# Kernel tuning notes

Hardware: AMD Instinct MI355X
Metric: run time of the kernel (lower is better)

Reference implementation:

```python
import jax, jax.numpy as jnp
import numpy as np

NUM_PATCHES = 16
QPB = 20          # qubits per tree block
NBLOCKS = 4
N = 1 << QPB      # 2**20 amplitudes per block statevector
INV_SQRT2 = 0.7071067811865476


def _single_qubit_states(x, pos_weights):
    """H @ (data-encoding rotations) |0> for every wire, grouped into blocks.
    x: (B,16,4,3) color angles; pos_weights: (16,2). Returns (B,4,20,2) c64.
    The leading Hadamard of the layer-1 IQP unitary is folded in here since
    the pre-layer-1 state is a tensor product of single-qubit states."""
    B = x.shape[0]
    hx, hy, hz = 0.5 * x[..., 0], 0.5 * x[..., 1], 0.5 * x[..., 2]
    v0 = jnp.cos(hx) + 0j
    v1 = -1j * jnp.sin(hx)                       # RX|0>
    cy, sy = jnp.cos(hy), jnp.sin(hy)
    w0 = cy * v0 - sy * v1
    w1 = sy * v0 + cy * v1                       # RY
    pz = jnp.exp(-1j * hz)
    w0 = pz * w0
    w1 = jnp.conj(pz) * w1                       # RZ
    color = jnp.stack([w0 + w1, w0 - w1], -1) * INV_SQRT2       # H  -> (B,16,4,2)

    px, py = 0.5 * pos_weights[:, 0], 0.5 * pos_weights[:, 1]
    a0 = jnp.cos(px) + 0j
    a1 = -1j * jnp.sin(px)                       # RX|0>
    cy, sy = jnp.cos(py), jnp.sin(py)
    b0 = cy * a0 - sy * a1
    b1 = sy * a0 + cy * a1                       # RY
    anc = jnp.stack([b0 + b1, b0 - b1], -1) * INV_SQRT2         # (16,2)
    anc = jnp.broadcast_to(anc[None, :, None, :], (B, NUM_PATCHES, 1, 2))

    states = jnp.concatenate([color, anc], axis=2)              # (B,16,5,2)
    return states.reshape(B, NBLOCKS, QPB, 2).astype(jnp.complex64)


def _forward(x, pos_weights, layer_1_weights, layer_2_weights, head_w, head_b):
    B = x.shape[0]
    states = _single_qubit_states(x, pos_weights)   # (B,4,20,2)

    # Build each block's 2^20 product statevector (wire 0 = slowest index).
    psi = states[:, :, 0, :]
    for q in range(1, QPB):
        psi = (psi[..., None] * states[:, :, q][:, :, None, :]).reshape(B, NBLOCKS, -1)

    # Layer-1 diagonal: RZ(a_i) + ring IsingZZ(b_i); phase exp(-i/2 (a.z + b.(z*roll(z)))).
    idx = jnp.arange(N, dtype=jnp.uint32)
    shifts = (QPB - 1 - jnp.arange(QPB, dtype=jnp.uint32))
    z = 1.0 - 2.0 * ((idx[None, :] >> shifts[:, None]) & 1).astype(jnp.float32)  # (20,N)
    a1, b1 = layer_1_weights[:, 0], layer_1_weights[:, 1]
    theta = a1 @ z + b1 @ (z * jnp.roll(z, -1, axis=0))
    psi = psi * jnp.exp(-0.5j * theta).astype(jnp.complex64)

    # Closing Hadamard layer of layer-1 IQP = Walsh-Hadamard transform on 20 wires.
    for i in range(QPB):
        psi = psi.reshape(B, NBLOCKS, 1 << i, 2, 1 << (QPB - 1 - i))
        p0, p1 = psi[:, :, :, 0, :], psi[:, :, :, 1, :]
        psi = jnp.stack([p0 + p1, p0 - p1], axis=3) * INV_SQRT2
    psi = psi.reshape(B, NBLOCKS, N)

    # Reduced density matrix on the 4 surviving qubits (first 4 wires) of each block.
    A = psi.reshape(B, NBLOCKS, 16, N // 16)
    rho4 = jnp.einsum('bkim,bkjm->bkij', A, jnp.conj(A))        # (B,4,16,16)
    r = rho4.reshape(B, NBLOCKS, 2, 2, 2, 2, 2, 2, 2, 2)
    rho012 = jnp.einsum('bkpqrxstux->bkpqrstu', r).reshape(B, NBLOCKS, 8, 8)
    rho123 = jnp.einsum('bkxpqrxstu->bkpqrstu', r).reshape(B, NBLOCKS, 8, 8)
    rho01  = jnp.einsum('bkpqxystxy->bkpqst', r).reshape(B, NBLOCKS, 4, 4)
    rho23  = jnp.einsum('bkxypqxyst->bkpqst', r).reshape(B, NBLOCKS, 4, 4)
    rho_q0 = jnp.einsum('bkpxyzqxyz->bkpq', r)                  # (B,4,2,2)
    rho_q3 = jnp.einsum('bkxyzpxyzq->bkpq', r)

    # Layer-2 IQP (H D H) in Heisenberg picture: U2^dag Z_k U2 =
    #   Z_k exp(-i a_k X_k) exp(-i b_{k-1} X_{k-1} X_k) exp(-i b_k X_k X_{k+1}),
    # a 3-qubit operator on ring positions (k-1, k, k+1) of the 16 survivors.
    I2 = jnp.eye(2, dtype=jnp.complex64)
    X = jnp.array([[0, 1], [1, 0]], dtype=jnp.complex64)
    Z = jnp.array([[1, 0], [0, -1]], dtype=jnp.complex64)
    I8 = jnp.eye(8, dtype=jnp.complex64)
    IZI = jnp.kron(I2, jnp.kron(Z, I2))
    IXI = jnp.kron(I2, jnp.kron(X, I2))
    XXI = jnp.kron(X, jnp.kron(X, I2))
    IXX = jnp.kron(I2, jnp.kron(X, X))

    def rot(t, P):
        return jnp.cos(t) * I8 - 1j * jnp.sin(t) * P

    a2, b2 = layer_2_weights[:, 0], layer_2_weights[:, 1]

    def heis_op(k):
        return IZI @ rot(a2[k], IXI) @ rot(b2[(k - 1) % 16], XXI) @ rot(b2[k], IXX)

    def tr(O, rho):  # Re Tr[O rho] per batch element
        return jnp.real(jnp.einsum('ij,bji->b', O, rho))

    # Blocks are independent before layer 2 -> cross-block joints are tensor products.
    # Ring position 15 = block 3 survivor q3; position 4 = block 1 survivor q0.
    rho_k0 = jnp.einsum('bij,bkl->bikjl', rho_q3[:, 3], rho01[:, 0]).reshape(B, 8, 8)
    rho_k3 = jnp.einsum('bij,bkl->bikjl', rho23[:, 0], rho_q0[:, 1]).reshape(B, 8, 8)

    e0 = tr(heis_op(0), rho_k0)
    e1 = tr(heis_op(1), rho012[:, 0])
    e2 = tr(heis_op(2), rho123[:, 0])
    e3 = tr(heis_op(3), rho_k3)
    q_out = jnp.stack([e0, e1, e2, e3], axis=-1).astype(jnp.float32)  # (B,4)

    out = q_out @ head_w.T + head_b
    norm = jnp.linalg.norm(out, axis=-1, keepdims=True)
    return out / jnp.maximum(norm, 1e-12)


def setup_inputs() -> dict:
    key = jax.random.key(0)
    ks = jax.random.split(key, 6)
    B = 8
    x = jax.random.uniform(ks[0], (B, NUM_PATCHES, 4, 3), dtype=jnp.float32,
                           minval=0.0, maxval=np.pi)
    pos_weights = jax.random.normal(ks[1], (16, 2), dtype=jnp.float32) * 0.01
    layer_1_weights = jax.random.normal(ks[2], (20, 2), dtype=jnp.float32) * 0.1
    layer_2_weights = jax.random.normal(ks[3], (16, 2), dtype=jnp.float32) * 0.1
    head_w = jax.random.normal(ks[4], (512, 4), dtype=jnp.float32) * 0.1
    head_b = jax.random.normal(ks[5], (512,), dtype=jnp.float32) * 0.01
    return {'x': x, 'pos_weights': pos_weights, 'layer_1_weights': layer_1_weights,
            'layer_2_weights': layer_2_weights, 'head_w': head_w, 'head_b': head_b}


def reference(x, pos_weights, layer_1_weights, layer_2_weights, head_w, head_b):
    return _forward(x, pos_weights, layer_1_weights, layer_2_weights, head_w, head_b)
```

## Files before the change

### kernel.cpp

```cpp
#include <hip/hip_runtime.h>
#include <math.h>

#define INV_SQRT2F 0.70710678118654752f

__device__ __forceinline__ float2 cmul(float2 a, float2 b) {
  return make_float2(a.x*b.x - a.y*b.y, a.x*b.y + a.y*b.x);
}
__device__ __forceinline__ float2 cmulc(float2 a, float2 b) {
  return make_float2(a.x*b.x + a.y*b.y, a.y*b.x - a.x*b.y);
}
__device__ __forceinline__ float2 cadd(float2 a, float2 b) {
  return make_float2(a.x + b.x, a.y + b.y);
}

__global__ __launch_bounds__(1024) void iqp_fused_kernel(
    const float* __restrict__ x,
    const float* __restrict__ pw,
    const float* __restrict__ lw,
    const float* __restrict__ l2,
    const float* __restrict__ hw,
    const float* __restrict__ hb,
    float* __restrict__ out)
{
  const int b = blockIdx.x;
  const int t = threadIdx.x;
  const int lane = t & 63;
  const int wid = t >> 6;

  __shared__ float2 sqs[3][20][2];
  __shared__ float  b1s[20];
  __shared__ float2 W[3][4][8][33];
  __shared__ float2 D0[8][64];
  __shared__ float2 ipv[6];
  __shared__ float2 q3part[4][3];
  __shared__ float2 rho[256];
  __shared__ float2 r012[64], r123[64], rk0[64], rk3[64];
  __shared__ float2 r01[16], r23[16], q0s[4], q3s[4];
  __shared__ float  e[4];
  __shared__ float  wsum[8];
  __shared__ float  nrm;

  if (t < 60) {
    const int kidx = t / 20, q = t % 20;
    const int k = (kidx == 2) ? 3 : kidx;
    const int pch = 4*k + q/5;
    const int j = q % 5;
    float2 s0, s1;
    if (j < 4) {
      const float* xp = x + ((size_t)((b*16 + pch)*4 + j))*3;
      float cx, sx, cy, sy, cz, sz;
      __sincosf(0.5f*xp[0], &sx, &cx);
      __sincosf(0.5f*xp[1], &sy, &cy);
      __sincosf(0.5f*xp[2], &sz, &cz);
      float2 w0 = make_float2(cy*cx,  sy*sx);
      float2 w1 = make_float2(sy*cx, -cy*sx);
      w0 = cmul(make_float2(cz, -sz), w0);
      w1 = cmul(make_float2(cz,  sz), w1);
      s0 = make_float2((w0.x + w1.x)*INV_SQRT2F, (w0.y + w1.y)*INV_SQRT2F);
      s1 = make_float2((w0.x - w1.x)*INV_SQRT2F, (w0.y - w1.y)*INV_SQRT2F);
    } else {
      float cx, sx, cy, sy;
      __sincosf(0.5f*pw[2*pch], &sx, &cx);
      __sincosf(0.5f*pw[2*pch + 1], &sy, &cy);
      const float2 w0 = make_float2(cy*cx,  sy*sx);
      const float2 w1 = make_float2(sy*cx, -cy*sx);
      s0 = make_float2((w0.x + w1.x)*INV_SQRT2F, (w0.y + w1.y)*INV_SQRT2F);
      s1 = make_float2((w0.x - w1.x)*INV_SQRT2F, (w0.y - w1.y)*INV_SQRT2F);
    }
    float ca, sa;
    __sincosf(0.5f*lw[2*q], &sa, &ca);
    sqs[kidx][q][0] = cmul(s0, make_float2(ca, -sa));
    sqs[kidx][q][1] = cmul(s1, make_float2(ca,  sa));
    if (kidx == 0) b1s[q] = lw[2*q + 1];
  }
  __syncthreads();

  if (wid < 12) {
    const int kk = wid >> 2;
    const int cls = wid & 3;
    const int b0 = cls & 1, b9 = cls >> 1;

    int bq[10];
    bq[0] = b0; bq[9] = b9;
    #pragma unroll
    for (int q = 3; q < 9; ++q) bq[q] = (lane >> (8 - q)) & 1;

    float2 base = sqs[kk][0][b0];
    #pragma unroll
    for (int q = 3; q < 9; ++q) base = cmul(base, sqs[kk][q][bq[q]]);
    base = cmul(base, sqs[kk][9][b9]);
    {
      float phi = 0.f;
      #pragma unroll
      for (int q = 3; q < 9; ++q) {
        const float zq  = 1.f - 2.f*(float)bq[q];
        const float zq1 = 1.f - 2.f*(float)bq[q + 1];
        phi += b1s[q]*zq*zq1;
      }
      float sp, cp;
      __sincosf(0.5f*phi, &sp, &cp);
      base = cmul(base, make_float2(cp, -sp));
    }
    const float2 t0 = cmul(base, sqs[kk][1][0]);
    const float2 t1 = cmul(base, sqs[kk][1][1]);
    const float z0 = 1.f - 2.f*(float)b0;
    const float z3 = 1.f - 2.f*(float)bq[3];

    float2 v[4];
    #pragma unroll
    for (int j = 0; j < 4; ++j) {
      const int j1 = j >> 1, j0 = j & 1;
      const float z1 = 1.f - 2.f*(float)j1;
      const float z2 = 1.f - 2.f*(float)j0;
      const float phij = b1s[0]*z0*z1 + b1s[1]*z1*z2 + b1s[2]*z2*z3;
      float sp, cp;
      __sincosf(0.5f*phij, &sp, &cp);
      v[j] = cmul(cmul(j1 ? t1 : t0, sqs[kk][2][j0]), make_float2(cp, -sp));
    }

    if (kk != 1) {
      {
        float2 a0 = v[0], a2 = v[2];
        v[0] = cadd(a0, a2); v[2] = make_float2(a0.x - a2.x, a0.y - a2.y);
        float2 a1 = v[1], a3 = v[3];
        v[1] = cadd(a1, a3); v[3] = make_float2(a1.x - a3.x, a1.y - a3.y);
        a0 = v[0]; a1 = v[1];
        v[0] = cadd(a0, a1); v[1] = make_float2(a0.x - a1.x, a0.y - a1.y);
        a2 = v[2]; a3 = v[3];
        v[2] = cadd(a2, a3); v[3] = make_float2(a2.x - a3.x, a2.y - a3.y);
      }
      #pragma unroll
      for (int mask = 1; mask <= 32; mask <<= 1) {
        #pragma unroll
        for (int j = 0; j < 4; ++j) {
          const float px = __shfl_xor(v[j].x, mask);
          const float py = __shfl_xor(v[j].y, mask);
          if (lane & mask) v[j] = make_float2(px - v[j].x, py - v[j].y);
          else             v[j] = make_float2(v[j].x + px, v[j].y + py);
        }
      }
    }
    const float scl = (kk == 1) ? 1.0f : 0.0625f;
    #pragma unroll
    for (int j = 0; j < 4; ++j) {
      const int m = j*64 + lane;
      W[kk][cls][m >> 5][m & 31] =
          make_float2(v[j].x*scl, v[j].y*scl);
    }
  }
  __syncthreads();

  if (wid < 8) {
    const int pr = t >> 6, idx = t & 63, xx = idx >> 3, yy = idx & 7;
    const int pa = pr >> 1;
    const int pb = (pr & 1) + ((pr >> 2) << 1);
    float2 acc = make_float2(0.f, 0.f);
    #pragma unroll 8
    for (int u = 0; u < 32; ++u)
      acc = cadd(acc, cmulc(W[0][pa][xx][u], W[0][pb][yy][u]));
    D0[pr][xx*8 + yy] = acc;
  } else if (wid < 12) {
    const int w4 = wid - 8;
    const int prl[6][2] = {{0,0},{1,1},{2,2},{3,3},{0,1},{2,3}};
    #pragma unroll
    for (int rep = 0; rep < 2; ++rep) {
      const int which = (rep == 0) ? w4 : w4 + 4;
      if (rep == 1 && w4 >= 2) break;
      const int pa = prl[which][0], pb = prl[which][1];
      float2 acc = make_float2(0.f, 0.f);
      #pragma unroll
      for (int jj = 0; jj < 4; ++jj) {
        const int m = jj*64 + lane;
        acc = cadd(acc, cmulc(W[1][pa][m >> 5][m & 31],
                              W[1][pb][m >> 5][m & 31]));
      }
      for (int off = 32; off > 0; off >>= 1) {
        acc.x += __shfl_down(acc.x, off);
        acc.y += __shfl_down(acc.y, off);
      }
      if (lane == 0) ipv[which] = acc;
    }
  } else {
    const int c = wid - 12;
    const int lo = lane >> 4;
    const int u0 = (lane & 15)*2;
    float2 a00 = make_float2(0.f, 0.f), a01 = a00, a11 = a00;
    #pragma unroll
    for (int du = 0; du < 2; ++du) {
      const float2 p0 = W[2][c][(lo << 1)    ][u0 + du];
      const float2 p1 = W[2][c][(lo << 1) | 1][u0 + du];
      a00 = cadd(a00, cmulc(p0, p0));
      a01 = cadd(a01, cmulc(p0, p1));
      a11 = cadd(a11, cmulc(p1, p1));
    }
    for (int off = 32; off > 0; off >>= 1) {
      a00.x += __shfl_down(a00.x, off); a00.y += __shfl_down(a00.y, off);
      a01.x += __shfl_down(a01.x, off); a01.y += __shfl_down(a01.y, off);
      a11.x += __shfl_down(a11.x, off); a11.y += __shfl_down(a11.y, off);
    }
    if (lane == 0) {
      q3part[c][0] = a00; q3part[c][1] = a01; q3part[c][2] = a11;
    }
  }
  __syncthreads();

  if (t < 256) {
    const int i = t >> 4, j = t & 15;
    const int xy = (i & 7)*8 + (j & 7);
    const int si = i >> 3, sj = j >> 3;
    const float2 q19a = sqs[0][19][0], q19b = sqs[0][19][1];
    const float s19a = q19a.x*q19a.x + q19a.y*q19a.y;
    const float s19b = q19b.x*q19b.x + q19b.y*q19b.y;
    const float cb = __cosf(b1s[19]), sb = __sinf(b1s[19]);
    const float2 gam = make_float2((s19a + s19b)*cb, (s19b - s19a)*sb);
    float2 acc = cadd(D0[0][xy], D0[4][xy]);
    {
      const float2 t2 = cadd(D0[3][xy], D0[7][xy]);
      const float sg = ((si ^ sj) & 1) ? -1.f : 1.f;
      acc.x += sg*t2.x; acc.y += sg*t2.y;
    }
    {
      float2 t3 = cadd(D0[1][xy], D0[5][xy]);
      t3 = cmul(gam, t3);
      const float sg = (sj & 1) ? -1.f : 1.f;
      acc.x += sg*t3.x; acc.y += sg*t3.y;
    }
    {
      float2 t4 = cadd(D0[2][xy], D0[6][xy]);
      t4 = cmulc(t4, gam);
      const float sg = (si & 1) ? -1.f : 1.f;
      acc.x += sg*t4.x; acc.y += sg*t4.y;
    }
    rho[t] = make_float2(0.5f*acc.x, 0.5f*acc.y);
  } else if (t < 260) {
    const int pp = (t - 256) >> 1, qq = (t - 256) & 1;
    const float2 q19a = sqs[1][19][0], q19b = sqs[1][19][1];
    const float s19a = q19a.x*q19a.x + q19a.y*q19a.y;
    const float s19b = q19b.x*q19b.x + q19b.y*q19b.y;
    const float cb = __cosf(b1s[19]), sb = __sinf(b1s[19]);
    const float2 gam1 = make_float2((s19a + s19b)*cb, (s19b - s19a)*sb);
    const float2 T04 = cadd(ipv[0], ipv[2]);
    const float2 T37 = cadd(ipv[1], ipv[3]);
    const float2 T15 = cadd(ipv[4], ipv[5]);
    const float2 h = cmul(gam1, T15);
    float2 acc = T04;
    const float sg1 = ((pp ^ qq) & 1) ? -1.f : 1.f;
    acc.x += sg1*T37.x; acc.y += sg1*T37.y;
    const float sgq = (qq & 1) ? -1.f : 1.f;
    acc.x += sgq*h.x; acc.y += sgq*h.y;
    const float sgp = (pp & 1) ? -1.f : 1.f;
    acc.x += sgp*h.x; acc.y -= sgp*h.y;
    q0s[pp*2 + qq] = make_float2(0.5f*acc.x, 0.5f*acc.y);
  } else if (t < 264) {
    const int ei = t - 260;
    const int pp = ei >> 1, qq = ei & 1;
    const int src = (pp == 0 && qq == 0) ? 0 : (pp == 1 && qq == 1) ? 2 : 1;
    float2 s = make_float2(0.f, 0.f);
    #pragma unroll
    for (int c = 0; c < 4; ++c) s = cadd(s, q3part[c][src]);
    if (pp == 1 && qq == 0) s.y = -s.y;
    q3s[pp*2 + qq] = s;
  }
  __syncthreads();

  if (t < 64) {
    const int i = t >> 3, j = t & 7;
    r012[t] = cadd(rho[(2*i)*16 + 2*j], rho[(2*i + 1)*16 + 2*j + 1]);
    r123[t] = cadd(rho[i*16 + j], rho[(i + 8)*16 + (j + 8)]);
  }
  if (t >= 64 && t < 80) {
    const int tt = t - 64;
    const int i = tt >> 2, j = tt & 3;
    float2 s1 = make_float2(0.f, 0.f), s2 = make_float2(0.f, 0.f);
    #pragma unroll
    for (int w = 0; w < 4; ++w) {
      s1 = cadd(s1, rho[(4*i + w)*16 + 4*j + w]);
      s2 = cadd(s2, rho[(4*w + i)*16 + 4*w + j]);
    }
    r01[tt] = s1;  r23[tt] = s2;
  }
  __syncthreads();

  if (t < 64) {
    const int i = t >> 3, j = t & 7;
    rk0[t] = cmul(q3s[(i >> 2)*2 + (j >> 2)], r01[(i & 3)*4 + (j & 3)]);
    rk3[t] = cmul(r23[(i >> 1)*4 + (j >> 1)], q0s[(i & 1)*2 + (j & 1)]);
  }
  __syncthreads();

  if (t < 256) {
    const int k = t >> 6;
    const int idx = t & 63;
    const int i = idx >> 3, j = idx & 7;
    const float alpha = l2[2*k];
    const float beta1 = l2[2*((k + 15) & 15) + 1];
    const float beta2 = l2[2*k + 1];
    float ca, sa, cb1, sb1, cb2, sb2;
    __sincosf(alpha, &sa, &ca);
    __sincosf(beta1, &sb1, &cb1);
    __sincosf(beta2, &sb2, &cb2);
    float2 m1, m2;
    {
      const int xr = i ^ j;
      m1 = (xr == 0) ? make_float2( cb1*cb2, 0.f)
         : (xr == 3) ? make_float2( 0.f,    -cb1*sb2)
         : (xr == 6) ? make_float2( 0.f,    -sb1*cb2)
         : (xr == 5) ? make_float2(-sb1*sb2, 0.f)
         : make_float2(0.f, 0.f);
      const int xr2 = xr ^ 2;
      m2 = (xr2 == 0) ? make_float2( cb1*cb2, 0.f)
         : (xr2 == 3) ? make_float2( 0.f,    -cb1*sb2)
         : (xr2 == 6) ? make_float2( 0.f,    -sb1*cb2)
         : (xr2 == 5) ? make_float2(-sb1*sb2, 0.f)
         : make_float2(0.f, 0.f);
    }
    float2 O = make_float2(ca*m1.x + sa*m2.y, ca*m1.y - sa*m2.x);
    if ((i >> 1) & 1) { O.x = -O.x; O.y = -O.y; }
    const float2* rp = (k == 0) ? rk0 : (k == 1) ? r012 : (k == 2) ? r123 : rk3;
    const float2 rv = rp[j*8 + i];
    float contrib = O.x*rv.x - O.y*rv.y;
    for (int off = 32; off > 0; off >>= 1) contrib += __shfl_down(contrib, off);
    if (idx == 0) e[k] = contrib;
  }
  __syncthreads();

  float val = 0.f;
  if (t < 512) {
    val = hb[t] + e[0]*hw[4*t] + e[1]*hw[4*t + 1]
        + e[2]*hw[4*t + 2] + e[3]*hw[4*t + 3];
    float ss = val*val;
    for (int off = 32; off > 0; off >>= 1) ss += __shfl_down(ss, off);
    if ((t & 63) == 0) wsum[t >> 6] = ss;
  }
  __syncthreads();
  if (t == 0) {
    float s = 0.f;
    for (int w = 0; w < 8; ++w) s += wsum[w];
    nrm = fmaxf(sqrtf(s), 1e-12f);
  }
  __syncthreads();
  if (t < 512) out[(size_t)b*512 + t] = val / nrm;
}

extern "C" void kernel_launch(void* const* d_in, const int* in_sizes, int n_in,
                              void* d_out, int out_size, void* d_ws, size_t ws_size,
                              hipStream_t stream) {
  const float* x  = (const float*)d_in[0];
  const float* pw = (const float*)d_in[1];
  const float* lw = (const float*)d_in[2];
  const float* l2 = (const float*)d_in[3];
  const float* hw = (const float*)d_in[4];
  const float* hb = (const float*)d_in[5];
  const int B = in_sizes[0] / (16*4*3);

  iqp_fused_kernel<<<B, 1024, 0, stream>>>(x, pw, lw, l2, hw, hb, (float*)d_out);
}
```

Before: 69.30 us.

## Shrink block to 768 threads, hoist trig/gamma precompute, merge partial-trace stages

```diff
diff --git a/kernel.cpp b/kernel.cpp
--- a/kernel.cpp
+++ b/kernel.cpp
@@ -13,7 +13,7 @@
   return make_float2(a.x + b.x, a.y + b.y);
 }
 
-__global__ __launch_bounds__(1024) void iqp_fused_kernel(
+__global__ __launch_bounds__(768) void iqp_fused_kernel(
     const float* __restrict__ x,
     const float* __restrict__ pw,
     const float* __restrict__ lw,
@@ -29,13 +29,15 @@
 
   __shared__ float2 sqs[3][20][2];
   __shared__ float  b1s[20];
+  __shared__ float2 gams[2];
+  __shared__ float  trig[4][6];
   __shared__ float2 W[3][4][8][33];
   __shared__ float2 D0[8][64];
   __shared__ float2 ipv[6];
   __shared__ float2 q3part[4][3];
   __shared__ float2 rho[256];
   __shared__ float2 r012[64], r123[64], rk0[64], rk3[64];
-  __shared__ float2 r01[16], r23[16], q0s[4], q3s[4];
+  __shared__ float2 q0s[4], q3s[4];
   __shared__ float  e[4];
   __shared__ float  wsum[8];
   __shared__ float  nrm;
@@ -72,10 +74,29 @@
     sqs[kidx][q][0] = cmul(s0, make_float2(ca, -sa));
     sqs[kidx][q][1] = cmul(s1, make_float2(ca,  sa));
     if (kidx == 0) b1s[q] = lw[2*q + 1];
-  }
-  __syncthreads();
-
-  if (wid < 12) {
+    if (q == 19 && kidx < 2) {
+      const float m0 = s0.x*s0.x + s0.y*s0.y;
+      const float m1 = s1.x*s1.x + s1.y*s1.y;
+      float sb, cb;
+      __sincosf(lw[39], &sb, &cb);
+      gams[kidx] = make_float2((m0 + m1)*cb, (m1 - m0)*sb);
+    }
+  } else if (t >= 64 && t < 68) {
+    const int k = t - 64;
+    const float alpha = l2[2*k];
+    const float beta1 = l2[2*((k + 15) & 15) + 1];
+    const float beta2 = l2[2*k + 1];
+    float ca, sa, cb1, sb1, cb2, sb2;
+    __sincosf(alpha, &sa, &ca);
+    __sincosf(beta1, &sb1, &cb1);
+    __sincosf(beta2, &sb2, &cb2);
+    trig[k][0] = ca;  trig[k][1] = sa;
+    trig[k][2] = cb1; trig[k][3] = sb1;
+    trig[k][4] = cb2; trig[k][5] = sb2;
+  }
+  __syncthreads();
+
+  {
     const int kk = wid >> 2;
     const int cls = wid & 3;
     const int b0 = cls & 1, b9 = cls >> 1;
@@ -159,13 +180,12 @@
     for (int u = 0; u < 32; ++u)
       acc = cadd(acc, cmulc(W[0][pa][xx][u], W[0][pb][yy][u]));
     D0[pr][xx*8 + yy] = acc;
-  } else if (wid < 12) {
-    const int w4 = wid - 8;
+  } else if (wid < 10) {
+    const int u = wid - 8;
     const int prl[6][2] = {{0,0},{1,1},{2,2},{3,3},{0,1},{2,3}};
     #pragma unroll
-    for (int rep = 0; rep < 2; ++rep) {
-      const int which = (rep == 0) ? w4 : w4 + 4;
-      if (rep == 1 && w4 >= 2) break;
+    for (int rep = 0; rep < 3; ++rep) {
+      const int which = u*3 + rep;
       const int pa = prl[which][0], pb = prl[which][1];
       float2 acc = make_float2(0.f, 0.f);
       #pragma unroll
@@ -181,25 +201,29 @@
       if (lane == 0) ipv[which] = acc;
     }
   } else {
-    const int c = wid - 12;
+    const int u = wid - 10;
     const int lo = lane >> 4;
     const int u0 = (lane & 15)*2;
-    float2 a00 = make_float2(0.f, 0.f), a01 = a00, a11 = a00;
-    #pragma unroll
-    for (int du = 0; du < 2; ++du) {
-      const float2 p0 = W[2][c][(lo << 1)    ][u0 + du];
-      const float2 p1 = W[2][c][(lo << 1) | 1][u0 + du];
-      a00 = cadd(a00, cmulc(p0, p0));
-      a01 = cadd(a01, cmulc(p0, p1));
-      a11 = cadd(a11, cmulc(p1, p1));
-    }
-    for (int off = 32; off > 0; off >>= 1) {
-      a00.x += __shfl_down(a00.x, off); a00.y += __shfl_down(a00.y, off);
-      a01.x += __shfl_down(a01.x, off); a01.y += __shfl_down(a01.y, off);
-      a11.x += __shfl_down(a11.x, off); a11.y += __shfl_down(a11.y, off);
-    }
-    if (lane == 0) {
-      q3part[c][0] = a00; q3part[c][1] = a01; q3part[c][2] = a11;
+    #pragma unroll
+    for (int cc = 0; cc < 2; ++cc) {
+      const int c = u*2 + cc;
+      float2 a00 = make_float2(0.f, 0.f), a01 = a00, a11 = a00;
+      #pragma unroll
+      for (int du = 0; du < 2; ++du) {
+        const float2 p0 = W[2][c][(lo << 1)    ][u0 + du];
+        const float2 p1 = W[2][c][(lo << 1) | 1][u0 + du];
+        a00 = cadd(a00, cmulc(p0, p0));
+        a01 = cadd(a01, cmulc(p0, p1));
+        a11 = cadd(a11, cmulc(p1, p1));
+      }
+      for (int off = 32; off > 0; off >>= 1) {
+        a00.x += __shfl_down(a00.x, off); a00.y += __shfl_down(a00.y, off);
+        a01.x += __shfl_down(a01.x, off); a01.y += __shfl_down(a01.y, off);
+        a11.x += __shfl_down(a11.x, off); a11.y += __shfl_down(a11.y, off);
+      }
+      if (lane == 0) {
+        q3part[c][0] = a00; q3part[c][1] = a01; q3part[c][2] = a11;
+      }
     }
   }
   __syncthreads();
@@ -208,11 +232,7 @@
     const int i = t >> 4, j = t & 15;
     const int xy = (i & 7)*8 + (j & 7);
     const int si = i >> 3, sj = j >> 3;
-    const float2 q19a = sqs[0][19][0], q19b = sqs[0][19][1];
-    const float s19a = q19a.x*q19a.x + q19a.y*q19a.y;
-    const float s19b = q19b.x*q19b.x + q19b.y*q19b.y;
-    const float cb = __cosf(b1s[19]), sb = __sinf(b1s[19]);
-    const float2 gam = make_float2((s19a + s19b)*cb, (s19b - s19a)*sb);
+    const float2 gam = gams[0];
     float2 acc = cadd(D0[0][xy], D0[4][xy]);
     {
       const float2 t2 = cadd(D0[3][xy], D0[7][xy]);
@@ -234,11 +254,7 @@
     rho[t] = make_float2(0.5f*acc.x, 0.5f*acc.y);
   } else if (t < 260) {
     const int pp = (t - 256) >> 1, qq = (t - 256) & 1;
-    const float2 q19a = sqs[1][19][0], q19b = sqs[1][19][1];
-    const float s19a = q19a.x*q19a.x + q19a.y*q19a.y;
-    const float s19b = q19b.x*q19b.x + q19b.y*q19b.y;
-    const float cb = __cosf(b1s[19]), sb = __sinf(b1s[19]);
-    const float2 gam1 = make_float2((s19a + s19b)*cb, (s19b - s19a)*sb);
+    const float2 gam1 = gams[1];
     const float2 T04 = cadd(ipv[0], ipv[2]);
     const float2 T37 = cadd(ipv[1], ipv[3]);
     const float2 T15 = cadd(ipv[4], ipv[5]);
@@ -267,24 +283,22 @@
     const int i = t >> 3, j = t & 7;
     r012[t] = cadd(rho[(2*i)*16 + 2*j], rho[(2*i + 1)*16 + 2*j + 1]);
     r123[t] = cadd(rho[i*16 + j], rho[(i + 8)*16 + (j + 8)]);
-  }
-  if (t >= 64 && t < 80) {
-    const int tt = t - 64;
-    const int i = tt >> 2, j = tt & 3;
-    float2 s1 = make_float2(0.f, 0.f), s2 = make_float2(0.f, 0.f);
-    #pragma unroll
-    for (int w = 0; w < 4; ++w) {
-      s1 = cadd(s1, rho[(4*i + w)*16 + 4*j + w]);
-      s2 = cadd(s2, rho[(4*w + i)*16 + 4*w + j]);
-    }
-    r01[tt] = s1;  r23[tt] = s2;
-  }
-  __syncthreads();
-
-  if (t < 64) {
-    const int i = t >> 3, j = t & 7;
-    rk0[t] = cmul(q3s[(i >> 2)*2 + (j >> 2)], r01[(i & 3)*4 + (j & 3)]);
-    rk3[t] = cmul(r23[(i >> 1)*4 + (j >> 1)], q0s[(i & 1)*2 + (j & 1)]);
+    {
+      const int ip = i & 3, jp = j & 3;
+      float2 s1 = make_float2(0.f, 0.f);
+      #pragma unroll
+      for (int w = 0; w < 4; ++w)
+        s1 = cadd(s1, rho[(4*ip + w)*16 + 4*jp + w]);
+      rk0[t] = cmul(q3s[(i >> 2)*2 + (j >> 2)], s1);
+    }
+    {
+      const int ip = i >> 1, jp = j >> 1;
+      float2 s2 = make_float2(0.f, 0.f);
+      #pragma unroll
+      for (int w = 0; w < 4; ++w)
+        s2 = cadd(s2, rho[(4*w + ip)*16 + 4*w + jp]);
+      rk3[t] = cmul(s2, q0s[(i & 1)*2 + (j & 1)]);
+    }
   }
   __syncthreads();
 
@@ -292,13 +306,9 @@
     const int k = t >> 6;
     const int idx = t & 63;
     const int i = idx >> 3, j = idx & 7;
-    const float alpha = l2[2*k];
-    const float beta1 = l2[2*((k + 15) & 15) + 1];
-    const float beta2 = l2[2*k + 1];
-    float ca, sa, cb1, sb1, cb2, sb2;
-    __sincosf(alpha, &sa, &ca);
-    __sincosf(beta1, &sb1, &cb1);
-    __sincosf(beta2, &sb2, &cb2);
+    const float ca  = trig[k][0], sa  = trig[k][1];
+    const float cb1 = trig[k][2], sb1 = trig[k][3];
+    const float cb2 = trig[k][4], sb2 = trig[k][5];
     float2 m1, m2;
     {
       const int xr = i ^ j;
@@ -353,5 +363,5 @@
   const float* hb = (const float*)d_in[5];
   const int B = in_sizes[0] / (16*4*3);
 
-  iqp_fused_kernel<<<B, 1024, 0, stream>>>(x, pw, lw, l2, hw, hb, (float*)d_out);
-}
+  iqp_fused_kernel<<<B, 768, 0, stream>>>(x, pw, lw, l2, hw, hb, (float*)d_out);
+}
```

Measured after the change: 69.27 us. About the same (-0.0%).
